# Kernel optimization log

Measured on AMD Instinct MI355X. Metric: run time of the kernel, lower is better.

Reference implementation:

```python
import jax, jax.numpy as jnp
import numpy as np

N_NODES = 20000
N_EDGES = 150000
IN_C = 512
OUT_C = 512
K_INIT = 7  # weight has K_INIT+1 = 8 slices, all used by the forward loop


def setup_inputs() -> dict:
    key = jax.random.key(0)
    k1, k2, k3, k4 = jax.random.split(key, 4)
    x = jax.random.normal(k1, (N_NODES, IN_C), dtype=jnp.float32)
    edge_index = jax.random.randint(k2, (2, N_EDGES), 0, N_NODES, dtype=jnp.int32)
    # uniform init as in reset_parameters: bound = 1/sqrt(in_channels * (K+1))
    bound = 1.0 / np.sqrt(IN_C * (K_INIT + 1))
    weight = jax.random.uniform(k3, (K_INIT + 1, IN_C, OUT_C), dtype=jnp.float32,
                                minval=-bound, maxval=bound)
    bias = jax.random.uniform(k4, (OUT_C,), dtype=jnp.float32,
                              minval=-bound, maxval=bound)
    return {"x": x, "edge_index": edge_index, "weight": weight, "bias": bias}


def _spmm(row, col, lap, x, num_nodes):
    # out[i] = sum_{e: row[e]==i} lap[e] * x[col[e]]
    msgs = lap[:, None] * x[col]  # [E, C] gather + scale
    return jax.ops.segment_sum(msgs, row, num_segments=num_nodes)


def reference(x, edge_index, weight, bias):
    row, col = edge_index[0], edge_index[1]
    num_nodes = x.shape[0]
    Kw = weight.shape[0]
    # degree^{-1/2} normalization of implicit adjacency, edge_attr = ones
    deg = jax.ops.segment_sum(jnp.ones_like(row, dtype=x.dtype), row,
                              num_segments=num_nodes)
    dinv = jnp.where(deg > 0, jax.lax.rsqrt(jnp.maximum(deg, 1e-30)), 0.0)
    lap = -dinv[row] * dinv[col]  # [E]
    Tx_0 = x
    out = Tx_0 @ weight[0]
    Tx_1 = _spmm(row, col, lap, x, num_nodes)
    out = out + Tx_1 @ weight[1]
    for k in range(2, Kw):
        Tx_2 = 2.0 * _spmm(row, col, lap, Tx_1, num_nodes) - Tx_0
        out = out + Tx_2 @ weight[k]
        Tx_0, Tx_1 = Tx_1, Tx_2
    return out + bias
```

## Files before the change

### kernel.cpp

```cpp
#include <hip/hip_runtime.h>

#define NN 20000
#define NP 20096
#define NE 150000
#define CC 512
#define KW 8
#define KT 4096
#define SCB 20

typedef __attribute__((ext_vector_type(8))) short short8;
typedef __attribute__((ext_vector_type(4))) float f32x4;
typedef __attribute__((ext_vector_type(4))) unsigned short ushort4v;
typedef __attribute__((ext_vector_type(8))) unsigned short ushort8v;

__device__ inline unsigned short f2bf(float f) {
  unsigned u = __builtin_bit_cast(unsigned, f);
  u += 0x7fffu + ((u >> 16) & 1u);
  return (unsigned short)(u >> 16);
}

__device__ inline float bf2f(unsigned short u) {
  return __builtin_bit_cast(float, (unsigned)u << 16);
}

__device__ inline void gload_lds16(const void* g, void* l) {
  __builtin_amdgcn_global_load_lds(
      (const __attribute__((address_space(1))) unsigned int*)g,
      (__attribute__((address_space(3))) unsigned int*)l, 16, 0, 0);
}


__global__ __launch_bounds__(256) void k_zero(int* __restrict__ deg, int* __restrict__ cursor) {
  int i = blockIdx.x * blockDim.x + threadIdx.x;
  if (i < NN) { deg[i] = 0; cursor[i] = 0; }
}

__global__ __launch_bounds__(256) void k_count(const int* __restrict__ row, int* __restrict__ deg) {
  int e = blockIdx.x * blockDim.x + threadIdx.x;
  if (e < NE) atomicAdd(&deg[row[e]], 1);
}

__global__ __launch_bounds__(256) void k_dinv(const int* __restrict__ deg, float* __restrict__ dinv) {
  int i = blockIdx.x * blockDim.x + threadIdx.x;
  if (i < NN) {
    int d = deg[i];
    dinv[i] = (d > 0) ? rsqrtf((float)d) : 0.0f;
  }
}

__global__ __launch_bounds__(1024) void k_scanA(const int* __restrict__ deg,
    int* __restrict__ row_off, int* __restrict__ bsum) {
  __shared__ int sm[1024];
  const int b = blockIdx.x, tid = threadIdx.x;
  int i = b * 1024 + tid;
  int v = (i < NN) ? deg[i] : 0;
  sm[tid] = v;
  __syncthreads();
  #pragma unroll
  for (int off = 1; off < 1024; off <<= 1) {
    int t = (tid >= off) ? sm[tid - off] : 0;
    __syncthreads();
    if (tid >= off) sm[tid] += t;
    __syncthreads();
  }
  if (i < NN) row_off[i] = sm[tid] - v;
  if (tid == 1023) bsum[b] = sm[1023];
}

__global__ __launch_bounds__(64) void k_scanB(int* __restrict__ bsum) {
  if (threadIdx.x == 0) {
    int run = 0;
    for (int b = 0; b < SCB; ++b) { int t = bsum[b]; bsum[b] = run; run += t; }
  }
}

__global__ __launch_bounds__(1024) void k_scanC(int* __restrict__ row_off, const int* __restrict__ bsum) {
  int i = blockIdx.x * 1024 + threadIdx.x;
  if (i < NN) row_off[i] += bsum[blockIdx.x];
  if (i == NN - 1) row_off[NN] = NE;
}

__global__ __launch_bounds__(256) void k_fill(const int* __restrict__ row, const int* __restrict__ col,
    const int* __restrict__ row_off, int* __restrict__ cursor, const float* __restrict__ dinv,
    int* __restrict__ csr_col, float* __restrict__ csr_val) {
  int e = blockIdx.x * blockDim.x + threadIdx.x;
  if (e < NE) {
    int r = row[e], c = col[e];
    int pos = row_off[r] + atomicAdd(&cursor[r], 1);
    csr_col[pos] = c;
    csr_val[pos] = -dinv[r] * dinv[c];
  }
}


__global__ __launch_bounds__(256) void k_wcast(const float* __restrict__ W, unsigned short* __restrict__ Bt) {
  __shared__ float sm[64][68];
  const int t = blockIdx.x;
  const int s = t >> 6;
  const int rem = t & 63;
  const int kt0 = (rem >> 3) * 64;
  const int nt0 = (rem & 7) * 64;
  const float* w = W + ((size_t)s << 18);
  const int tid = threadIdx.x;
  #pragma unroll
  for (int i = 0; i < 4; ++i) {
    int f = tid + i * 256;
    int r = f >> 4;
    int c4 = f & 15;
    float4 v = *(const float4*)&w[(size_t)(kt0 + r) * CC + nt0 + c4 * 4];
    sm[r][c4 * 4 + 0] = v.x; sm[r][c4 * 4 + 1] = v.y;
    sm[r][c4 * 4 + 2] = v.z; sm[r][c4 * 4 + 3] = v.w;
  }
  __syncthreads();
  #pragma unroll
  for (int i = 0; i < 2; ++i) {
    int g = tid + i * 256;
    int nl = g >> 3;
    int k8 = (g & 7) * 8;
    ushort8v o;
    #pragma unroll
    for (int j = 0; j < 8; ++j) o[j] = f2bf(sm[k8 + j][nl]);
    *(ushort8v*)&Bt[(size_t)(nt0 + nl) * KT + s * CC + kt0 + k8] = o;
  }
}

__global__ __launch_bounds__(256) void k_xcast(const float* __restrict__ x, unsigned short* __restrict__ txall) {
  size_t t = (size_t)blockIdx.x * 256 + threadIdx.x;
  size_t idx = t * 8;
  if (idx >= (size_t)NN * CC) return;
  size_t r = idx >> 9;
  int c = (int)(idx & 511);
  const float4* p = (const float4*)&x[idx];
  float4 a = p[0], b = p[1];
  ushort8v v;
  v[0] = f2bf(a.x); v[1] = f2bf(a.y); v[2] = f2bf(a.z); v[3] = f2bf(a.w);
  v[4] = f2bf(b.x); v[5] = f2bf(b.y); v[6] = f2bf(b.z); v[7] = f2bf(b.w);
  *(ushort8v*)&txall[r * KT + c] = v;
}


__global__ __launch_bounds__(256) void k_spmm(const unsigned short* __restrict__ gsrc,
    const unsigned short* __restrict__ gprev, unsigned short* __restrict__ gdst,
    const int* __restrict__ row_off, const int* __restrict__ csr_col,
    const float* __restrict__ csr_val, float alpha, float beta)
{
  const int tid = threadIdx.x;
  const int i = blockIdx.x * 4 + (tid >> 6);
  const int c8 = (tid & 63) * 8;
  const int e0 = row_off[i];
  const int e1 = row_off[i + 1];

  float a0[8] = {}, a1[8] = {}, a2[8] = {}, a3[8] = {};
  int e = e0;
  for (; e + 3 < e1; e += 4) {
    int j0 = csr_col[e], j1 = csr_col[e+1], j2 = csr_col[e+2], j3 = csr_col[e+3];
    float v0 = csr_val[e], v1 = csr_val[e+1], v2 = csr_val[e+2], v3 = csr_val[e+3];
    const ushort8v x0 = *(const ushort8v*)&gsrc[(size_t)j0 * KT + c8];
    const ushort8v x1 = *(const ushort8v*)&gsrc[(size_t)j1 * KT + c8];
    const ushort8v x2 = *(const ushort8v*)&gsrc[(size_t)j2 * KT + c8];
    const ushort8v x3 = *(const ushort8v*)&gsrc[(size_t)j3 * KT + c8];
    #pragma unroll
    for (int q = 0; q < 8; ++q) {
      a0[q] += v0 * bf2f(x0[q]);
      a1[q] += v1 * bf2f(x1[q]);
      a2[q] += v2 * bf2f(x2[q]);
      a3[q] += v3 * bf2f(x3[q]);
    }
  }
  for (; e < e1; ++e) {
    int j = csr_col[e];
    float v = csr_val[e];
    const ushort8v xv = *(const ushort8v*)&gsrc[(size_t)j * KT + c8];
    #pragma unroll
    for (int q = 0; q < 8; ++q) a0[q] += v * bf2f(xv[q]);
  }

  ushort8v bv;
  if (beta != 0.0f) {
    const ushort8v p = *(const ushort8v*)&gprev[(size_t)i * KT + c8];
    #pragma unroll
    for (int q = 0; q < 8; ++q) {
      float s = (a0[q] + a1[q]) + (a2[q] + a3[q]);
      bv[q] = f2bf(alpha * s + beta * bf2f(p[q]));
    }
  } else {
    #pragma unroll
    for (int q = 0; q < 8; ++q) {
      float s = (a0[q] + a1[q]) + (a2[q] + a3[q]);
      bv[q] = f2bf(alpha * s);
    }
  }
  *(ushort8v*)&gdst[(size_t)i * KT + c8] = bv;
}


__global__ __launch_bounds__(256) void k_gemm(const unsigned short* __restrict__ A,
    const unsigned short* __restrict__ Bt, float* __restrict__ C,
    const float* __restrict__ bias)
{
  __shared__ unsigned short smA[128 * 32];
  __shared__ unsigned short smB[64 * 32];
  const int tid  = threadIdx.x;
  const int lane = tid & 63;
  const int wave = tid >> 6;
  const int wr = wave >> 1, wc = wave & 1;

  int bid = blockIdx.x;
  int wgid = (bid & 7) * 157 + (bid >> 3);
  const int m0 = (wgid >> 3) * 128;
  const int n0 = (wgid & 7) * 64;

  const int srow = lane >> 2;
  const int skc  = (lane & 3) * 8;

  f32x4 acc[4][2] = {};

  for (int k0 = 0; k0 < KT; k0 += 32) {
    #pragma unroll
    for (int i = 0; i < 2; ++i) {
      int row = wave * 32 + i * 16;
      gload_lds16(&A[(size_t)(m0 + row + srow) * KT + k0 + skc], &smA[row * 32]);
    }
    {
      int row = wave * 16;
      gload_lds16(&Bt[(size_t)(n0 + row + srow) * KT + k0 + skc], &smB[row * 32]);
    }
    __syncthreads();

    short8 af[4], bfv[2];
    #pragma unroll
    for (int f = 0; f < 4; ++f)
      af[f]  = *(const short8*)&smA[(wr * 64 + f * 16 + (lane & 15)) * 32 + (lane >> 4) * 8];
    #pragma unroll
    for (int f = 0; f < 2; ++f)
      bfv[f] = *(const short8*)&smB[(wc * 32 + f * 16 + (lane & 15)) * 32 + (lane >> 4) * 8];
    #pragma unroll
    for (int fm = 0; fm < 4; ++fm)
      #pragma unroll
      for (int fn = 0; fn < 2; ++fn)
        acc[fm][fn] = __builtin_amdgcn_mfma_f32_16x16x32_bf16(af[fm], bfv[fn], acc[fm][fn], 0, 0, 0);
    __syncthreads();
  }

  const int prow = (lane >> 4) * 4;
  const int pcol = lane & 15;
  #pragma unroll
  for (int fm = 0; fm < 4; ++fm) {
    #pragma unroll
    for (int fn = 0; fn < 2; ++fn) {
      int gcol = n0 + wc * 32 + fn * 16 + pcol;
      float bb = bias[gcol];
      #pragma unroll
      for (int j = 0; j < 4; ++j) {
        int grow = m0 + wr * 64 + fm * 16 + prow + j;
        if (grow < NN) C[(size_t)grow * CC + gcol] = acc[fm][fn][j] + bb;
      }
    }
  }
}


extern "C" void kernel_launch(void* const* d_in, const int* in_sizes, int n_in,
                              void* d_out, int out_size, void* d_ws, size_t ws_size,
                              hipStream_t stream) {
  const float* x      = (const float*)d_in[0];
  const int*   row    = (const int*)d_in[1];
  const int*   col    = row + NE;
  const float* weight = (const float*)d_in[2];
  const float* bias   = (const float*)d_in[3];
  float* out = (float*)d_out;

  unsigned short* TxAll = (unsigned short*)d_ws;
  unsigned short* Bt    = TxAll + (size_t)NP * KT;
  float* dinv    = (float*)(Bt + (size_t)CC * KT);
  float* csr_val = dinv + NN;
  int*   deg     = (int*)(csr_val + NE);
  int*   cursor  = deg + NN;
  int*   row_off = cursor + NN;
  int*   csr_col = row_off + NN + 1;
  int*   bsum    = csr_col + NE;

  k_zero<<<(NN + 255) / 256, 256, 0, stream>>>(deg, cursor);
  k_count<<<(NE + 255) / 256, 256, 0, stream>>>(row, deg);
  k_dinv<<<(NN + 255) / 256, 256, 0, stream>>>(deg, dinv);
  k_scanA<<<SCB, 1024, 0, stream>>>(deg, row_off, bsum);
  k_scanB<<<1, 64, 0, stream>>>(bsum);
  k_scanC<<<SCB, 1024, 0, stream>>>(row_off, bsum);
  k_fill<<<(NE + 255) / 256, 256, 0, stream>>>(row, col, row_off, cursor, dinv, csr_col, csr_val);

  k_wcast<<<512, 256, 0, stream>>>(weight, Bt);
  k_xcast<<<(NN * CC / 8 + 255) / 256, 256, 0, stream>>>(x, TxAll);

  const int spmm_grid = NN / 4;
  k_spmm<<<spmm_grid, 256, 0, stream>>>(TxAll, TxAll, TxAll + CC, row_off, csr_col, csr_val, 1.0f, 0.0f);
  for (int k = 2; k < KW; ++k)
    k_spmm<<<spmm_grid, 256, 0, stream>>>(TxAll + (size_t)(k - 1) * CC, TxAll + (size_t)(k - 2) * CC,
                                          TxAll + (size_t)k * CC, row_off, csr_col, csr_val, 2.0f, -1.0f);

  k_gemm<<<157 * 8, 256, 0, stream>>>(TxAll, Bt, out, bias);
}
```

Before: 382.4 us.

## Batch SpMM neighbor gathers by eight and enlarge GEMM tile to 128x128 with 8 waves

The SpMM kernel now issues eight neighbor-row gathers per iteration with masked tail handling and a single accumulator, instead of four unrolled gathers plus a scalar remainder loop. This is meant to raise memory-level parallelism on the irregular gathers. The GEMM moves to 512-thread blocks computing 128x128 output tiles, so there are fewer blocks and less redundant A loading, and it uses an XCD-aware workgroup remap. In exchange, SpMM register pressure grows and padded iterations load wasted rows for low-degree nodes.

```diff
diff --git a/kernel.cpp b/kernel.cpp
--- a/kernel.cpp
+++ b/kernel.cpp
@@ -150,65 +150,63 @@
   const int e0 = row_off[i];
   const int e1 = row_off[i + 1];
 
-  float a0[8] = {}, a1[8] = {}, a2[8] = {}, a3[8] = {};
-  int e = e0;
-  for (; e + 3 < e1; e += 4) {
-    int j0 = csr_col[e], j1 = csr_col[e+1], j2 = csr_col[e+2], j3 = csr_col[e+3];
-    float v0 = csr_val[e], v1 = csr_val[e+1], v2 = csr_val[e+2], v3 = csr_val[e+3];
-    const ushort8v x0 = *(const ushort8v*)&gsrc[(size_t)j0 * KT + c8];
-    const ushort8v x1 = *(const ushort8v*)&gsrc[(size_t)j1 * KT + c8];
-    const ushort8v x2 = *(const ushort8v*)&gsrc[(size_t)j2 * KT + c8];
-    const ushort8v x3 = *(const ushort8v*)&gsrc[(size_t)j3 * KT + c8];
+  float acc[8] = {};
+  for (int base = e0; base < e1; base += 8) {
+    int   idxs[8];
+    float vals[8];
     #pragma unroll
     for (int q = 0; q < 8; ++q) {
-      a0[q] += v0 * bf2f(x0[q]);
-      a1[q] += v1 * bf2f(x1[q]);
-      a2[q] += v2 * bf2f(x2[q]);
-      a3[q] += v3 * bf2f(x3[q]);
+      int ee = base + q;
+      bool ok = ee < e1;
+      int ec = ok ? ee : (e1 - 1);
+      idxs[q] = csr_col[ec];
+      vals[q] = ok ? csr_val[ec] : 0.0f;
     }
-  }
-  for (; e < e1; ++e) {
-    int j = csr_col[e];
-    float v = csr_val[e];
-    const ushort8v xv = *(const ushort8v*)&gsrc[(size_t)j * KT + c8];
-    #pragma unroll
-    for (int q = 0; q < 8; ++q) a0[q] += v * bf2f(xv[q]);
+    ushort8v xs[8];
+    #pragma unroll
+    for (int q = 0; q < 8; ++q)
+      xs[q] = *(const ushort8v*)&gsrc[(size_t)idxs[q] * KT + c8];
+    #pragma unroll
+    for (int q = 0; q < 8; ++q)
+      #pragma unroll
+      for (int p = 0; p < 8; ++p)
+        acc[p] += vals[q] * bf2f(xs[q][p]);
   }
 
   ushort8v bv;
   if (beta != 0.0f) {
     const ushort8v p = *(const ushort8v*)&gprev[(size_t)i * KT + c8];
     #pragma unroll
-    for (int q = 0; q < 8; ++q) {
-      float s = (a0[q] + a1[q]) + (a2[q] + a3[q]);
-      bv[q] = f2bf(alpha * s + beta * bf2f(p[q]));
-    }
+    for (int q = 0; q < 8; ++q)
+      bv[q] = f2bf(alpha * acc[q] + beta * bf2f(p[q]));
   } else {
     #pragma unroll
-    for (int q = 0; q < 8; ++q) {
-      float s = (a0[q] + a1[q]) + (a2[q] + a3[q]);
-      bv[q] = f2bf(alpha * s);
-    }
+    for (int q = 0; q < 8; ++q)
+      bv[q] = f2bf(alpha * acc[q]);
   }
   *(ushort8v*)&gdst[(size_t)i * KT + c8] = bv;
 }
 
 
-__global__ __launch_bounds__(256) void k_gemm(const unsigned short* __restrict__ A,
+__global__ __launch_bounds__(512) void k_gemm(const unsigned short* __restrict__ A,
     const unsigned short* __restrict__ Bt, float* __restrict__ C,
     const float* __restrict__ bias)
 {
   __shared__ unsigned short smA[128 * 32];
-  __shared__ unsigned short smB[64 * 32];
+  __shared__ unsigned short smB[128 * 32];
   const int tid  = threadIdx.x;
   const int lane = tid & 63;
   const int wave = tid >> 6;
-  const int wr = wave >> 1, wc = wave & 1;
-
+  const int wr = wave >> 2;
+  const int wc = wave & 3;
+
+  const int nwg = (NP / 128) * 4;
   int bid = blockIdx.x;
-  int wgid = (bid & 7) * 157 + (bid >> 3);
-  const int m0 = (wgid >> 3) * 128;
-  const int n0 = (wgid & 7) * 64;
+  int q = nwg >> 3, rr = nwg & 7;
+  int xcd = bid & 7, lid = bid >> 3;
+  int wgid = (xcd < rr ? xcd * (q + 1) : rr * (q + 1) + (xcd - rr) * q) + lid;
+  const int m0 = (wgid >> 2) * 128;
+  const int n0 = (wgid & 3) * 128;
 
   const int srow = lane >> 2;
   const int skc  = (lane & 3) * 8;
@@ -216,13 +214,9 @@
   f32x4 acc[4][2] = {};
 
   for (int k0 = 0; k0 < KT; k0 += 32) {
-    #pragma unroll
-    for (int i = 0; i < 2; ++i) {
-      int row = wave * 32 + i * 16;
-      gload_lds16(&A[(size_t)(m0 + row + srow) * KT + k0 + skc], &smA[row * 32]);
-    }
     {
       int row = wave * 16;
+      gload_lds16(&A[(size_t)(m0 + row + srow) * KT + k0 + skc], &smA[row * 32]);
       gload_lds16(&Bt[(size_t)(n0 + row + srow) * KT + k0 + skc], &smB[row * 32]);
     }
     __syncthreads();
@@ -297,5 +291,5 @@
     k_spmm<<<spmm_grid, 256, 0, stream>>>(TxAll + (size_t)(k - 1) * CC, TxAll + (size_t)(k - 2) * CC,
                                           TxAll + (size_t)k * CC, row_off, csr_col, csr_val, 2.0f, -1.0f);
 
-  k_gemm<<<157 * 8, 256, 0, stream>>>(TxAll, Bt, out, bias);
-}
+  k_gemm<<<(NP / 128) * 4, 512, 0, stream>>>(TxAll, Bt, out, bias);
+}
```

After: 347.2 us. 1.1x faster.
